# Kernel optimization log

Hardware: AMD Instinct MI355X
Metric: run time of the kernel (lower is better)

Reference implementation:

```python
import jax, jax.numpy as jnp
import numpy as np

B, GH, GW, F = 64, 7, 7, 1024  # batch, enc grid, feature_size (hardcoded 1024 in module)
A, E, H, V, T = 512, 512, 512, 30000, 20  # attention_dim, embed, hidden, vocab, max caption len


def setup_inputs() -> dict:
    key = jax.random.key(0)
    ks = jax.random.split(key, 20)
    s = 0.02
    features = jax.random.normal(ks[0], (B, GH, GW, F), jnp.float32)
    captions = jax.random.randint(ks[1], (B, T), 0, V)
    lengths = jax.random.randint(ks[2], (B,), 2, T + 1)
    lengths = lengths.at[0].set(T)  # ensure max(decode_lengths) == T-1 (static)
    inp = dict(features=features, captions=captions, lengths=lengths)
    inp["We"] = jax.random.normal(ks[3], (A, F), jnp.float32) * s   # attention.encoder_att
    inp["be"] = jnp.zeros((A,), jnp.float32)
    inp["Wd"] = jax.random.normal(ks[4], (A, H), jnp.float32) * s   # attention.decoder_att
    inp["bd"] = jnp.zeros((A,), jnp.float32)
    inp["Wf"] = jax.random.normal(ks[5], (1, A), jnp.float32) * s   # attention.full_att
    inp["bf"] = jnp.zeros((1,), jnp.float32)
    inp["emb"] = jax.random.uniform(ks[6], (V, E), jnp.float32, -0.1, 0.1)
    inp["Wih"] = jax.random.normal(ks[7], (3 * H, E + F), jnp.float32) * s  # GRUCell weight_ih
    inp["Whh"] = jax.random.normal(ks[8], (3 * H, H), jnp.float32) * s      # GRUCell weight_hh
    inp["bih"] = jnp.zeros((3 * H,), jnp.float32)
    inp["bhh"] = jnp.zeros((3 * H,), jnp.float32)
    inp["Winit"] = jax.random.normal(ks[9], (H, F), jnp.float32) * s  # init_h
    inp["binit"] = jnp.zeros((H,), jnp.float32)
    inp["Wbeta"] = jax.random.normal(ks[10], (F, H), jnp.float32) * s  # f_beta
    inp["bbeta"] = jnp.zeros((F,), jnp.float32)
    inp["Wfc"] = jax.random.uniform(ks[11], (V, H), jnp.float32, -0.1, 0.1)  # fc
    inp["bfc"] = jnp.zeros((V,), jnp.float32)
    return inp


def reference(features, captions, lengths, We, be, Wd, bd, Wf, bf, emb,
              Wih, Whh, bih, bhh, Winit, binit, Wbeta, bbeta, Wfc, bfc):
    b = features.shape[0]
    feats = features.reshape(b, -1, features.shape[-1])  # (B, P, F)
    sort_ind = jnp.argsort(-lengths)
    lengths_s = lengths[sort_ind]
    feats = feats[sort_ind]
    caps = captions[sort_ind]
    decode_lengths = lengths_s - 1
    Tm = captions.shape[1] - 1  # static max decode length (lengths max == T)

    embs = emb[caps]                                  # (B, T, E)
    h0 = feats.mean(axis=1) @ Winit.T + binit         # (B, H)
    att1 = feats @ We.T + be                          # (B, P, A), loop-invariant

    def step(h, xs):
        emb_t, active = xs  # (B,E), (B,)
        att2 = h @ Wd.T + bd                                  # (B, A)
        e = jax.nn.relu(att1 + att2[:, None, :]) @ Wf[0] + bf[0]  # (B, P)
        alpha = jax.nn.softmax(e, axis=1)
        awe = jnp.einsum('bpf,bp->bf', feats, alpha)          # (B, F)
        gate = jax.nn.sigmoid(h @ Wbeta.T + bbeta)
        x = jnp.concatenate([emb_t, gate * awe], axis=1)      # (B, E+F)
        gi = x @ Wih.T + bih
        gh = h @ Whh.T + bhh
        ir, iz, inn = jnp.split(gi, 3, axis=1)
        hr, hz, hn = jnp.split(gh, 3, axis=1)
        r = jax.nn.sigmoid(ir + hr)
        z = jax.nn.sigmoid(iz + hz)
        n = jnp.tanh(inn + r * hn)
        h_new = (1.0 - z) * n + z * h
        preds = h_new @ Wfc.T + bfc                           # dropout in eval = identity
        am = active[:, None]
        return jnp.where(am, h_new, h), (jnp.where(am, preds, 0.0), jnp.where(am, alpha, 0.0))

    ts = jnp.arange(Tm)
    active = ts[:, None] < decode_lengths[None, :]            # (Tm, B)
    emb_seq = jnp.swapaxes(embs[:, :Tm, :], 0, 1)             # (Tm, B, E)
    _, (preds, alphas) = jax.lax.scan(step, h0, (emb_seq, active))
    predictions = jnp.swapaxes(preds, 0, 1)                   # (B, Tm, V)
    alphas = jnp.swapaxes(alphas, 0, 1)                       # (B, Tm, P)
    return predictions, caps, decode_lengths, alphas, sort_ind
```

## Files before the change

### kernel.cpp

```cpp
#include <hip/hip_runtime.h>
#include <math.h>

typedef __attribute__((ext_vector_type(8))) short bf16x8;
typedef __attribute__((ext_vector_type(4))) float f32x4;

#define TM 19
#define NV 30000

__device__ __forceinline__ float bf2f(unsigned short u){
  union { unsigned int i; float f; } v; v.i = ((unsigned int)u) << 16; return v.f;
}
__device__ __forceinline__ unsigned short f2bf(float f){
  union { float f; unsigned int i; } v; v.f = f;
  unsigned int x = v.i;
  unsigned int r = (x + 0x7fffu + ((x >> 16) & 1u)) >> 16;
  return (unsigned short)r;
}

__global__ void k_sort(const int* __restrict__ lengths, const int* __restrict__ captions,
                       int* __restrict__ sort_ws, int* __restrict__ dl_ws, int* __restrict__ caps_ws,
                       float* __restrict__ out_caps, float* __restrict__ out_dl, float* __restrict__ out_sort){
  int b = threadIdx.x;
  __shared__ int len_s[64];
  len_s[b] = lengths[b];
  __syncthreads();
  int lb = len_s[b];
  int r = 0;
  for(int j = 0; j < 64; j++){
    int lj = len_s[j];
    r += (lj > lb) || (lj == lb && j < b);
  }
  sort_ws[r] = b;
  dl_ws[r] = lb - 1;
  out_sort[r] = (float)b;
  out_dl[r] = (float)(lb - 1);
  for(int tt = 0; tt < 20; tt++){
    int c = captions[b*20 + tt];
    caps_ws[r*20 + tt] = c;
    out_caps[r*20 + tt] = (float)c;
  }
}

__global__ void k_cvt4(const float4* __restrict__ src, ushort4* __restrict__ dst, int n4){
  int i = blockIdx.x*256 + threadIdx.x;
  if(i < n4){
    float4 v = src[i];
    ushort4 o; o.x = f2bf(v.x); o.y = f2bf(v.y); o.z = f2bf(v.z); o.w = f2bf(v.w);
    dst[i] = o;
  }
}

__global__ void k_feats(const float* __restrict__ feats, const int* __restrict__ sort_ws,
                        unsigned short* __restrict__ feats_bf){
  int rp = blockIdx.x;
  int r = rp / 49, p = rp % 49;
  int sb = sort_ws[r];
  const float* src = feats + ((size_t)sb*49 + p)*1024;
  unsigned short* dst = feats_bf + (size_t)rp*1024;
  int f = threadIdx.x*4;
  float4 v = *(const float4*)(src + f);
  ushort4 o; o.x = f2bf(v.x); o.y = f2bf(v.y); o.z = f2bf(v.z); o.w = f2bf(v.w);
  *(ushort4*)(dst + f) = o;
}

__global__ void k_featmean(const float* __restrict__ feats, const int* __restrict__ sort_ws,
                           float* __restrict__ fm){
  int r = blockIdx.x;
  int sb = sort_ws[r];
  const float* src = feats + (size_t)sb*49*1024;
  int f = threadIdx.x*4;
  float a0=0,a1=0,a2=0,a3=0;
  for(int p = 0; p < 49; p++){
    float4 v = *(const float4*)(src + p*1024 + f);
    a0 += v.x; a1 += v.y; a2 += v.z; a3 += v.w;
  }
  const float inv = 1.0f/49.0f;
  float4 o; o.x=a0*inv; o.y=a1*inv; o.z=a2*inv; o.w=a3*inv;
  *(float4*)(fm + r*1024 + f) = o;
}

__global__ void k_h0(const float* __restrict__ fm, const float* __restrict__ Winit,
                     const float* __restrict__ binit,
                     float* __restrict__ h, unsigned short* __restrict__ h_bf){
  int idx = blockIdx.x*256 + threadIdx.x;
  int r = idx >> 9, n = idx & 511;
  const float* a = fm + r*1024;
  const float* wrow = Winit + (size_t)n*1024;
  float s = 0.f;
  for(int k = 0; k < 1024; k += 4){
    float4 av = *(const float4*)(a + k);
    float4 wv = *(const float4*)(wrow + k);
    s += av.x*wv.x + av.y*wv.y + av.z*wv.z + av.w*wv.w;
  }
  s += binit[n];
  h[idx] = s;
  h_bf[idx] = f2bf(s);
}

__global__ void k_embs(const float* __restrict__ emb, const int* __restrict__ caps_ws,
                       unsigned short* __restrict__ embs_bf){
  int row = blockIdx.x;
  int t = row >> 6, r = row & 63;
  int cap = caps_ws[r*20 + t];
  const float* src = emb + (size_t)cap*512;
  unsigned short* dst = embs_bf + (size_t)row*512;
  int e = threadIdx.x*2;
  float2 v = *(const float2*)(src + e);
  dst[e]   = f2bf(v.x);
  dst[e+1] = f2bf(v.y);
}

__global__ __launch_bounds__(256) void k_gemm64(
    const unsigned short* __restrict__ A, int lda,
    const unsigned short* __restrict__ Bm, int ldb,
    float* __restrict__ C, int ldc, int Ksplit){
  __shared__ unsigned short As[64*40];
  __shared__ unsigned short Bs[64*40];
  int tid = threadIdx.x;
  int wave = tid >> 6, lane = tid & 63;
  int m0 = blockIdx.y*64, n0 = blockIdx.x*64;
  int k0 = blockIdx.z*Ksplit;
  int lrow = tid >> 2, lcol = (tid & 3)*8;
  const unsigned short* Ag = A + (size_t)(m0 + lrow)*lda + k0 + lcol;
  const unsigned short* Bg = Bm + (size_t)(n0 + lrow)*ldb + k0 + lcol;
  f32x4 acc0 = {0,0,0,0}, acc1 = {0,0,0,0}, acc2 = {0,0,0,0}, acc3 = {0,0,0,0};
  int quad = lane >> 4;
  int mrow = (wave << 4) + (lane & 15);
  for(int kk = 0; kk < Ksplit; kk += 32){
    uint4 av = *(const uint4*)(Ag + kk);
    uint4 bv = *(const uint4*)(Bg + kk);
    __syncthreads();
    *(uint4*)(&As[lrow*40 + lcol]) = av;
    *(uint4*)(&Bs[lrow*40 + lcol]) = bv;
    __syncthreads();
    bf16x8 a = *(const bf16x8*)(&As[mrow*40 + quad*8]);
    bf16x8 b0 = *(const bf16x8*)(&Bs[( 0 + (lane & 15))*40 + quad*8]);
    bf16x8 b1 = *(const bf16x8*)(&Bs[(16 + (lane & 15))*40 + quad*8]);
    bf16x8 b2 = *(const bf16x8*)(&Bs[(32 + (lane & 15))*40 + quad*8]);
    bf16x8 b3 = *(const bf16x8*)(&Bs[(48 + (lane & 15))*40 + quad*8]);
    acc0 = __builtin_amdgcn_mfma_f32_16x16x32_bf16(a, b0, acc0, 0, 0, 0);
    acc1 = __builtin_amdgcn_mfma_f32_16x16x32_bf16(a, b1, acc1, 0, 0, 0);
    acc2 = __builtin_amdgcn_mfma_f32_16x16x32_bf16(a, b2, acc2, 0, 0, 0);
    acc3 = __builtin_amdgcn_mfma_f32_16x16x32_bf16(a, b3, acc3, 0, 0, 0);
  }
  float* Cb = C + (size_t)blockIdx.z * ((size_t)gridDim.y*64*ldc);
  int col = lane & 15;
  #pragma unroll
  for(int rg = 0; rg < 4; rg++){
    int m = m0 + (wave << 4) + quad*4 + rg;
    float* crow = Cb + (size_t)m*ldc + n0 + col;
    crow[0]  = acc0[rg];
    crow[16] = acc1[rg];
    crow[32] = acc2[rg];
    crow[48] = acc3[rg];
  }
}

__global__ __launch_bounds__(256) void k_attn(
    const float* __restrict__ att1, const float* __restrict__ y1p,
    const float* __restrict__ bd, const float* __restrict__ be,
    const float* __restrict__ Wf, const float* __restrict__ bfb,
    const float* __restrict__ bbeta,
    const unsigned short* __restrict__ feats_bf,
    const int* __restrict__ dl_ws,
    unsigned short* __restrict__ x_awe, float* __restrict__ out_alph, int t){
  int r = blockIdx.x;
  int tid = threadIdx.x;
  __shared__ float att2s[512];
  __shared__ float es[64];
  __shared__ float alph[49];
  const float* y0 = y1p + (size_t)r*3072;
  const float* y1 = y1p + (size_t)64*3072 + (size_t)r*3072;
  for(int k = tid; k < 512; k += 256) att2s[k] = y0[k] + y1[k] + bd[k] + be[k];
  __syncthreads();
  int wave = tid >> 6, lane = tid & 63;
  for(int p = wave; p < 49; p += 4){
    const float* arow = att1 + ((size_t)r*49 + p)*512;
    float s = 0.f;
    #pragma unroll
    for(int i = 0; i < 8; i++){
      int k = lane + i*64;
      float v = arow[k] + att2s[k];
      s += fmaxf(v, 0.f) * Wf[k];
    }
    #pragma unroll
    for(int off = 32; off; off >>= 1) s += __shfl_xor(s, off, 64);
    if(lane == 0) es[p] = s + bfb[0];
  }
  __syncthreads();
  if(wave == 0){
    float v = (lane < 49) ? es[lane] : -1e30f;
    float m = v;
    #pragma unroll
    for(int off = 32; off; off >>= 1) m = fmaxf(m, __shfl_xor(m, off, 64));
    float ex = (lane < 49) ? __expf(v - m) : 0.f;
    float sm = ex;
    #pragma unroll
    for(int off = 32; off; off >>= 1) sm += __shfl_xor(sm, off, 64);
    float al = ex / sm;
    if(lane < 49){
      alph[lane] = al;
      bool act = t < dl_ws[r];
      out_alph[(size_t)r*(TM*49) + t*49 + lane] = act ? al : 0.f;
    }
  }
  __syncthreads();
  int f0 = tid*4;
  float a0=0,a1=0,a2=0,a3=0;
  const unsigned short* fr = feats_bf + (size_t)r*49*1024 + f0;
  for(int p = 0; p < 49; p++){
    float al = alph[p];
    ushort4 v = *(const ushort4*)(fr + p*1024);
    a0 += al*bf2f(v.x); a1 += al*bf2f(v.y); a2 += al*bf2f(v.z); a3 += al*bf2f(v.w);
  }
  const float* g0 = y0 + 512;
  const float* g1 = y1 + 512;
  ushort4 xo;
  float gp;
  gp = g0[f0+0] + g1[f0+0] + bbeta[f0+0]; xo.x = f2bf(a0 / (1.f + __expf(-gp)));
  gp = g0[f0+1] + g1[f0+1] + bbeta[f0+1]; xo.y = f2bf(a1 / (1.f + __expf(-gp)));
  gp = g0[f0+2] + g1[f0+2] + bbeta[f0+2]; xo.z = f2bf(a2 / (1.f + __expf(-gp)));
  gp = g0[f0+3] + g1[f0+3] + bbeta[f0+3]; xo.w = f2bf(a3 / (1.f + __expf(-gp)));
  *(ushort4*)(x_awe + (size_t)r*1024 + f0) = xo;
}

__global__ __launch_bounds__(256) void k_gru(
    const float* __restrict__ gi_emb, const float* __restrict__ gip,
    const float* __restrict__ y1p,
    const float* __restrict__ bih, const float* __restrict__ bhh,
    const int* __restrict__ dl_ws,
    float* __restrict__ h, unsigned short* __restrict__ h_bf,
    unsigned short* __restrict__ hseq, int t){
  int idx = blockIdx.x*256 + threadIdx.x;
  int r = idx >> 9, j = idx & 511;
  const float* ge = gi_emb + (size_t)(t*64 + r)*1536;
  float ir = ge[j], iz = ge[512 + j], in_ = ge[1024 + j];
  #pragma unroll
  for(int s = 0; s < 4; s++){
    const float* gp = gip + (size_t)s*64*1536 + (size_t)r*1536;
    ir += gp[j]; iz += gp[512 + j]; in_ += gp[1024 + j];
  }
  ir += bih[j]; iz += bih[512 + j]; in_ += bih[1024 + j];
  float hr = bhh[j], hz = bhh[512 + j], hn = bhh[1024 + j];
  #pragma unroll
  for(int s = 0; s < 2; s++){
    const float* yp = y1p + (size_t)s*64*3072 + (size_t)r*3072 + 1536;
    hr += yp[j]; hz += yp[512 + j]; hn += yp[1024 + j];
  }
  float rg = 1.f / (1.f + __expf(-(ir + hr)));
  float zg = 1.f / (1.f + __expf(-(iz + hz)));
  float ng = tanhf(in_ + rg*hn);
  float hold = h[idx];
  float hnew = (1.f - zg)*ng + zg*hold;
  hseq[(size_t)t*32768 + idx] = f2bf(hnew);
  bool act = t < dl_ws[r];
  float hout = act ? hnew : hold;
  h[idx] = hout;
  h_bf[idx] = f2bf(hout);
}

__global__ __launch_bounds__(256) void k_preds(
    const unsigned short* __restrict__ hseq, const unsigned short* __restrict__ Wfc_bf,
    const float* __restrict__ bfc, const int* __restrict__ dl_ws,
    float* __restrict__ out_pred){
  __shared__ unsigned short As[64*40];
  __shared__ unsigned short Bs[64*40];
  int tid = threadIdx.x;
  int wave = tid >> 6, lane = tid & 63;
  int m0 = blockIdx.y*64, n0 = blockIdx.x*64;
  int lrow = tid >> 2, lcol = (tid & 3)*8;
  const unsigned short* Ag = hseq + (size_t)(m0 + lrow)*512 + lcol;
  int brow = n0 + lrow;
  bool bvalid = brow < NV;
  const unsigned short* Bg = Wfc_bf + (size_t)(bvalid ? brow : 0)*512 + lcol;
  f32x4 acc0 = {0,0,0,0}, acc1 = {0,0,0,0}, acc2 = {0,0,0,0}, acc3 = {0,0,0,0};
  int quad = lane >> 4;
  int mrow = (wave << 4) + (lane & 15);
  for(int kk = 0; kk < 512; kk += 32){
    uint4 av = *(const uint4*)(Ag + kk);
    uint4 bv;
    if(bvalid) bv = *(const uint4*)(Bg + kk);
    else { bv.x = 0; bv.y = 0; bv.z = 0; bv.w = 0; }
    __syncthreads();
    *(uint4*)(&As[lrow*40 + lcol]) = av;
    *(uint4*)(&Bs[lrow*40 + lcol]) = bv;
    __syncthreads();
    bf16x8 a = *(const bf16x8*)(&As[mrow*40 + quad*8]);
    bf16x8 b0 = *(const bf16x8*)(&Bs[( 0 + (lane & 15))*40 + quad*8]);
    bf16x8 b1 = *(const bf16x8*)(&Bs[(16 + (lane & 15))*40 + quad*8]);
    bf16x8 b2 = *(const bf16x8*)(&Bs[(32 + (lane & 15))*40 + quad*8]);
    bf16x8 b3 = *(const bf16x8*)(&Bs[(48 + (lane & 15))*40 + quad*8]);
    acc0 = __builtin_amdgcn_mfma_f32_16x16x32_bf16(a, b0, acc0, 0, 0, 0);
    acc1 = __builtin_amdgcn_mfma_f32_16x16x32_bf16(a, b1, acc1, 0, 0, 0);
    acc2 = __builtin_amdgcn_mfma_f32_16x16x32_bf16(a, b2, acc2, 0, 0, 0);
    acc3 = __builtin_amdgcn_mfma_f32_16x16x32_bf16(a, b3, acc3, 0, 0, 0);
  }
  int col = lane & 15;
  #pragma unroll
  for(int j = 0; j < 4; j++){
    int n = n0 + j*16 + col;
    if(n < NV){
      float bias = bfc[n];
      f32x4 acc = (j == 0) ? acc0 : (j == 1) ? acc1 : (j == 2) ? acc2 : acc3;
      #pragma unroll
      for(int rg = 0; rg < 4; rg++){
        int mr = m0 + (wave << 4) + quad*4 + rg;
        int t = mr >> 6, r = mr & 63;
        bool act = t < dl_ws[r];
        float v = act ? (acc[rg] + bias) : 0.f;
        out_pred[(size_t)r*((size_t)TM*NV) + (size_t)t*NV + n] = v;
      }
    }
  }
}

extern "C" void kernel_launch(void* const* d_in, const int* in_sizes, int n_in,
                              void* d_out, int out_size, void* d_ws, size_t ws_size,
                              hipStream_t stream){
  const float* features = (const float*)d_in[0];
  const int*   captions = (const int*)d_in[1];
  const int*   lengths  = (const int*)d_in[2];
  const float* We    = (const float*)d_in[3];
  const float* be    = (const float*)d_in[4];
  const float* Wd    = (const float*)d_in[5];
  const float* bd    = (const float*)d_in[6];
  const float* Wf    = (const float*)d_in[7];
  const float* bfb   = (const float*)d_in[8];
  const float* emb   = (const float*)d_in[9];
  const float* Wih   = (const float*)d_in[10];
  const float* Whh   = (const float*)d_in[11];
  const float* bih   = (const float*)d_in[12];
  const float* bhh   = (const float*)d_in[13];
  const float* Winit = (const float*)d_in[14];
  const float* binit = (const float*)d_in[15];
  const float* Wbeta = (const float*)d_in[16];
  const float* bbeta = (const float*)d_in[17];
  const float* Wfc   = (const float*)d_in[18];
  const float* bfc   = (const float*)d_in[19];

  float* out = (float*)d_out;
  float* out_pred = out;
  float* out_caps = out + 36480000;
  float* out_dl   = out + 36481280;
  float* out_alph = out + 36481344;
  float* out_sort = out + 36540928;

  char* w = (char*)d_ws;
  auto alloc = [&](size_t bytes){ void* p = (void*)w; w += (bytes + 255) & ~(size_t)255; return p; };
  unsigned short* We_bf    = (unsigned short*)alloc((size_t)512*1024*2);
  unsigned short* W1_bf    = (unsigned short*)alloc((size_t)3072*512*2);
  unsigned short* Wih_bf   = (unsigned short*)alloc((size_t)1536*1536*2);
  unsigned short* Wfc_bf   = (unsigned short*)alloc((size_t)NV*512*2);
  unsigned short* feats_bf = (unsigned short*)alloc((size_t)64*49*1024*2);
  unsigned short* embs_bf  = (unsigned short*)alloc((size_t)1216*512*2);
  unsigned short* hseq_bf  = (unsigned short*)alloc((size_t)1216*512*2);
  unsigned short* h_bf     = (unsigned short*)alloc((size_t)64*512*2);
  unsigned short* xawe_bf  = (unsigned short*)alloc((size_t)64*1024*2);
  float* att1   = (float*)alloc((size_t)3136*512*4);
  float* gi_emb = (float*)alloc((size_t)1216*1536*4);
  float* y1p    = (float*)alloc((size_t)2*64*3072*4);
  float* gip    = (float*)alloc((size_t)4*64*1536*4);
  float* hbuf   = (float*)alloc((size_t)64*512*4);
  float* fmean  = (float*)alloc((size_t)64*1024*4);
  int* sort_ws  = (int*)alloc(64*4);
  int* dl_ws    = (int*)alloc(64*4);
  int* caps_ws  = (int*)alloc(1280*4);
  (void)in_sizes; (void)n_in; (void)out_size; (void)ws_size;

  k_sort<<<1, 64, 0, stream>>>(lengths, captions, sort_ws, dl_ws, caps_ws, out_caps, out_dl, out_sort);

  k_cvt4<<<512,  256, 0, stream>>>((const float4*)We,    (ushort4*)We_bf,             512*1024/4);
  k_cvt4<<<256,  256, 0, stream>>>((const float4*)Wd,    (ushort4*)W1_bf,             512*512/4);
  k_cvt4<<<512,  256, 0, stream>>>((const float4*)Wbeta, (ushort4*)(W1_bf + 512*512), 1024*512/4);
  k_cvt4<<<768,  256, 0, stream>>>((const float4*)Whh,   (ushort4*)(W1_bf + 1536*512),1536*512/4);
  k_cvt4<<<2304, 256, 0, stream>>>((const float4*)Wih,   (ushort4*)Wih_bf,            1536*1536/4);
  k_cvt4<<<15000,256, 0, stream>>>((const float4*)Wfc,   (ushort4*)Wfc_bf,            NV*512/4);

  k_feats<<<3136, 256, 0, stream>>>(features, sort_ws, feats_bf);
  k_featmean<<<64, 256, 0, stream>>>(features, sort_ws, fmean);
  k_h0<<<128, 256, 0, stream>>>(fmean, Winit, binit, hbuf, h_bf);
  k_embs<<<1216, 256, 0, stream>>>(emb, caps_ws, embs_bf);

  k_gemm64<<<dim3(8, 49, 1), 256, 0, stream>>>(feats_bf, 1024, We_bf, 1024, att1, 512, 1024);
  k_gemm64<<<dim3(24, 19, 1), 256, 0, stream>>>(embs_bf, 512, Wih_bf, 1536, gi_emb, 1536, 512);

  for(int t = 0; t < TM; t++){
    k_gemm64<<<dim3(48, 1, 2), 256, 0, stream>>>(h_bf, 512, W1_bf, 512, y1p, 3072, 256);
    k_attn<<<64, 256, 0, stream>>>(att1, y1p, bd, be, Wf, bfb, bbeta, feats_bf, dl_ws, xawe_bf, out_alph, t);
    k_gemm64<<<dim3(24, 1, 4), 256, 0, stream>>>(xawe_bf, 1024, Wih_bf + 512, 1536, gip, 1536, 256);
    k_gru<<<128, 256, 0, stream>>>(gi_emb, gip, y1p, bih, bhh, dl_ws, hbuf, h_bf, hseq_bf, t);
  }

  k_preds<<<dim3(469, 19, 1), 256, 0, stream>>>(hseq_bf, Wfc_bf, bfc, dl_ws, out_pred);
}
```

Before: 943.2 us.

## Fuse recurrent decode loop into one persistent kernel with grid barriers

Replaces the 76 per-timestep kernel launches (gemm, attention, gemm, GRU) with a single persistent kernel of 96 blocks. The blocks step through the four phases and sync at atomic-counter grid barriers. The goal is to remove launch overhead and inter-kernel gaps on the serial recurrence. The final prediction GEMM grid is also transposed so adjacent blocks share the same Wfc tile. The persistent kernel relies on all 96 blocks being co-resident, and leaves many blocks idle during the attention phase.

```diff
diff --git a/kernel.cpp b/kernel.cpp
--- a/kernel.cpp
+++ b/kernel.cpp
@@ -6,6 +6,7 @@
 
 #define TM 19
 #define NV 30000
+#define NB 96
 
 __device__ __forceinline__ float bf2f(unsigned short u){
   union { unsigned int i; float f; } v; v.i = ((unsigned int)u) << 16; return v.f;
@@ -17,10 +18,26 @@
   return (unsigned short)r;
 }
 
+__device__ __forceinline__ void gbar(int* cnt, int& phase){
+  __syncthreads();
+  if(threadIdx.x == 0){
+    phase++;
+    __threadfence();
+    __hip_atomic_fetch_add(cnt, 1, __ATOMIC_RELEASE, __HIP_MEMORY_SCOPE_AGENT);
+    while(__hip_atomic_load(cnt, __ATOMIC_ACQUIRE, __HIP_MEMORY_SCOPE_AGENT) < NB*phase){
+      __builtin_amdgcn_s_sleep(1);
+    }
+    __threadfence();
+  }
+  __syncthreads();
+}
+
 __global__ void k_sort(const int* __restrict__ lengths, const int* __restrict__ captions,
                        int* __restrict__ sort_ws, int* __restrict__ dl_ws, int* __restrict__ caps_ws,
-                       float* __restrict__ out_caps, float* __restrict__ out_dl, float* __restrict__ out_sort){
+                       float* __restrict__ out_caps, float* __restrict__ out_dl, float* __restrict__ out_sort,
+                       int* __restrict__ cnt){
   int b = threadIdx.x;
+  if(b == 0) *cnt = 0;
   __shared__ int len_s[64];
   len_s[b] = lengths[b];
   __syncthreads();
@@ -110,25 +127,22 @@
   dst[e+1] = f2bf(v.y);
 }
 
-__global__ __launch_bounds__(256) void k_gemm64(
+__device__ __forceinline__ void gemm64_dev(
     const unsigned short* __restrict__ A, int lda,
-    const unsigned short* __restrict__ Bm, int ldb,
-    float* __restrict__ C, int ldc, int Ksplit){
-  __shared__ unsigned short As[64*40];
-  __shared__ unsigned short Bs[64*40];
+    const unsigned short* __restrict__ B, int ldb,
+    float* __restrict__ C, int ldc, int kiters,
+    unsigned short* As, unsigned short* Bs){
   int tid = threadIdx.x;
   int wave = tid >> 6, lane = tid & 63;
-  int m0 = blockIdx.y*64, n0 = blockIdx.x*64;
-  int k0 = blockIdx.z*Ksplit;
   int lrow = tid >> 2, lcol = (tid & 3)*8;
-  const unsigned short* Ag = A + (size_t)(m0 + lrow)*lda + k0 + lcol;
-  const unsigned short* Bg = Bm + (size_t)(n0 + lrow)*ldb + k0 + lcol;
+  const unsigned short* Ag = A + (size_t)lrow*lda + lcol;
+  const unsigned short* Bg = B + (size_t)lrow*ldb + lcol;
   f32x4 acc0 = {0,0,0,0}, acc1 = {0,0,0,0}, acc2 = {0,0,0,0}, acc3 = {0,0,0,0};
   int quad = lane >> 4;
   int mrow = (wave << 4) + (lane & 15);
-  for(int kk = 0; kk < Ksplit; kk += 32){
-    uint4 av = *(const uint4*)(Ag + kk);
-    uint4 bv = *(const uint4*)(Bg + kk);
+  for(int it = 0; it < kiters; it++){
+    uint4 av = *(const uint4*)(Ag + it*32);
+    uint4 bv = *(const uint4*)(Bg + it*32);
     __syncthreads();
     *(uint4*)(&As[lrow*40 + lcol]) = av;
     *(uint4*)(&Bs[lrow*40 + lcol]) = bv;
@@ -143,12 +157,11 @@
     acc2 = __builtin_amdgcn_mfma_f32_16x16x32_bf16(a, b2, acc2, 0, 0, 0);
     acc3 = __builtin_amdgcn_mfma_f32_16x16x32_bf16(a, b3, acc3, 0, 0, 0);
   }
-  float* Cb = C + (size_t)blockIdx.z * ((size_t)gridDim.y*64*ldc);
   int col = lane & 15;
   #pragma unroll
   for(int rg = 0; rg < 4; rg++){
-    int m = m0 + (wave << 4) + quad*4 + rg;
-    float* crow = Cb + (size_t)m*ldc + n0 + col;
+    int m = (wave << 4) + quad*4 + rg;
+    float* crow = C + (size_t)m*ldc + col;
     crow[0]  = acc0[rg];
     crow[16] = acc1[rg];
     crow[32] = acc2[rg];
@@ -156,107 +169,143 @@
   }
 }
 
-__global__ __launch_bounds__(256) void k_attn(
-    const float* __restrict__ att1, const float* __restrict__ y1p,
-    const float* __restrict__ bd, const float* __restrict__ be,
-    const float* __restrict__ Wf, const float* __restrict__ bfb,
-    const float* __restrict__ bbeta,
-    const unsigned short* __restrict__ feats_bf,
-    const int* __restrict__ dl_ws,
-    unsigned short* __restrict__ x_awe, float* __restrict__ out_alph, int t){
-  int r = blockIdx.x;
+__global__ __launch_bounds__(256) void k_gemm64(
+    const unsigned short* __restrict__ A, int lda,
+    const unsigned short* __restrict__ Bm, int ldb,
+    float* __restrict__ C, int ldc, int Ksplit){
+  __shared__ unsigned short As[64*40];
+  __shared__ unsigned short Bs[64*40];
+  int m0 = blockIdx.y*64, n0 = blockIdx.x*64;
+  int k0 = blockIdx.z*Ksplit;
+  float* Cb = C + (size_t)blockIdx.z * ((size_t)gridDim.y*64*ldc);
+  gemm64_dev(A + (size_t)m0*lda + k0, lda, Bm + (size_t)n0*ldb + k0, ldb,
+             Cb + (size_t)m0*ldc + n0, ldc, Ksplit/32, As, Bs);
+}
+
+__global__ __launch_bounds__(256) void k_loop(
+    const float* __restrict__ att1, const float* __restrict__ bd, const float* __restrict__ be,
+    const float* __restrict__ Wf, const float* __restrict__ bfb, const float* __restrict__ bbeta,
+    const unsigned short* __restrict__ feats_bf, const int* __restrict__ dl_ws,
+    const unsigned short* __restrict__ W1_bf, const unsigned short* __restrict__ Wih_bf,
+    const float* __restrict__ gi_emb, const float* __restrict__ bih, const float* __restrict__ bhh,
+    float* __restrict__ y1p, float* __restrict__ gip,
+    unsigned short* __restrict__ xawe_bf,
+    float* __restrict__ h, unsigned short* __restrict__ h_bf, unsigned short* __restrict__ hseq,
+    float* __restrict__ out_alph, int* cnt){
+  __shared__ __align__(16) char smbuf[10240];
+  unsigned short* As = (unsigned short*)smbuf;
+  unsigned short* Bs = (unsigned short*)(smbuf + 5120);
+  float* att2s = (float*)smbuf;
+  float* es    = (float*)(smbuf + 2048);
+  float* alph  = (float*)(smbuf + 2304);
+  int blk = blockIdx.x;
   int tid = threadIdx.x;
-  __shared__ float att2s[512];
-  __shared__ float es[64];
-  __shared__ float alph[49];
-  const float* y0 = y1p + (size_t)r*3072;
-  const float* y1 = y1p + (size_t)64*3072 + (size_t)r*3072;
-  for(int k = tid; k < 512; k += 256) att2s[k] = y0[k] + y1[k] + bd[k] + be[k];
-  __syncthreads();
-  int wave = tid >> 6, lane = tid & 63;
-  for(int p = wave; p < 49; p += 4){
-    const float* arow = att1 + ((size_t)r*49 + p)*512;
-    float s = 0.f;
-    #pragma unroll
-    for(int i = 0; i < 8; i++){
-      int k = lane + i*64;
-      float v = arow[k] + att2s[k];
-      s += fmaxf(v, 0.f) * Wf[k];
-    }
-    #pragma unroll
-    for(int off = 32; off; off >>= 1) s += __shfl_xor(s, off, 64);
-    if(lane == 0) es[p] = s + bfb[0];
-  }
-  __syncthreads();
-  if(wave == 0){
-    float v = (lane < 49) ? es[lane] : -1e30f;
-    float m = v;
-    #pragma unroll
-    for(int off = 32; off; off >>= 1) m = fmaxf(m, __shfl_xor(m, off, 64));
-    float ex = (lane < 49) ? __expf(v - m) : 0.f;
-    float sm = ex;
-    #pragma unroll
-    for(int off = 32; off; off >>= 1) sm += __shfl_xor(sm, off, 64);
-    float al = ex / sm;
-    if(lane < 49){
-      alph[lane] = al;
+  int phase = 0;
+
+  for(int t = 0; t < TM; t++){
+    {
+      int tile = blk % 48, ks = blk / 48;
+      int n0 = tile*64, k0 = ks*256;
+      gemm64_dev(h_bf + k0, 512, W1_bf + (size_t)n0*512 + k0, 512,
+                 y1p + (size_t)ks*64*3072 + n0, 3072, 8, As, Bs);
+    }
+    gbar(cnt, phase);
+
+    if(blk < 64){
+      int r = blk;
+      int wave = tid >> 6, lane = tid & 63;
+      const float* y0 = y1p + (size_t)r*3072;
+      const float* y1 = y1p + (size_t)64*3072 + (size_t)r*3072;
+      for(int k = tid; k < 512; k += 256) att2s[k] = y0[k] + y1[k] + bd[k] + be[k];
+      __syncthreads();
+      for(int p = wave; p < 49; p += 4){
+        const float* arow = att1 + ((size_t)r*49 + p)*512;
+        float s = 0.f;
+        #pragma unroll
+        for(int i = 0; i < 8; i++){
+          int k = lane + i*64;
+          float v = arow[k] + att2s[k];
+          s += fmaxf(v, 0.f) * Wf[k];
+        }
+        #pragma unroll
+        for(int off = 32; off; off >>= 1) s += __shfl_xor(s, off, 64);
+        if(lane == 0) es[p] = s + bfb[0];
+      }
+      __syncthreads();
+      if(wave == 0){
+        float v = (lane < 49) ? es[lane] : -1e30f;
+        float m = v;
+        #pragma unroll
+        for(int off = 32; off; off >>= 1) m = fmaxf(m, __shfl_xor(m, off, 64));
+        float ex = (lane < 49) ? __expf(v - m) : 0.f;
+        float sm = ex;
+        #pragma unroll
+        for(int off = 32; off; off >>= 1) sm += __shfl_xor(sm, off, 64);
+        float al = ex / sm;
+        if(lane < 49){
+          alph[lane] = al;
+          bool act = t < dl_ws[r];
+          out_alph[(size_t)r*(TM*49) + t*49 + lane] = act ? al : 0.f;
+        }
+      }
+      __syncthreads();
+      int f0 = tid*4;
+      float a0=0,a1=0,a2=0,a3=0;
+      const unsigned short* fr = feats_bf + (size_t)r*49*1024 + f0;
+      for(int p = 0; p < 49; p++){
+        float al = alph[p];
+        ushort4 v = *(const ushort4*)(fr + p*1024);
+        a0 += al*bf2f(v.x); a1 += al*bf2f(v.y); a2 += al*bf2f(v.z); a3 += al*bf2f(v.w);
+      }
+      const float* g0 = y0 + 512;
+      const float* g1 = y1 + 512;
+      ushort4 xo;
+      float gp;
+      gp = g0[f0+0] + g1[f0+0] + bbeta[f0+0]; xo.x = f2bf(a0 / (1.f + __expf(-gp)));
+      gp = g0[f0+1] + g1[f0+1] + bbeta[f0+1]; xo.y = f2bf(a1 / (1.f + __expf(-gp)));
+      gp = g0[f0+2] + g1[f0+2] + bbeta[f0+2]; xo.z = f2bf(a2 / (1.f + __expf(-gp)));
+      gp = g0[f0+3] + g1[f0+3] + bbeta[f0+3]; xo.w = f2bf(a3 / (1.f + __expf(-gp)));
+      *(ushort4*)(xawe_bf + (size_t)r*1024 + f0) = xo;
+    }
+    gbar(cnt, phase);
+
+    {
+      int tile = blk % 24, ks = blk / 24;
+      int n0 = tile*64, k0 = ks*256;
+      gemm64_dev(xawe_bf + k0, 1024, Wih_bf + 512 + (size_t)n0*1536 + k0, 1536,
+                 gip + (size_t)ks*64*1536 + n0, 1536, 8, As, Bs);
+    }
+    gbar(cnt, phase);
+
+    for(int idx = blk*256 + tid; idx < 32768; idx += NB*256){
+      int r = idx >> 9, j = idx & 511;
+      const float* ge = gi_emb + (size_t)(t*64 + r)*1536;
+      float ir = ge[j], iz = ge[512 + j], in_ = ge[1024 + j];
+      #pragma unroll
+      for(int s = 0; s < 4; s++){
+        const float* gp = gip + (size_t)s*64*1536 + (size_t)r*1536;
+        ir += gp[j]; iz += gp[512 + j]; in_ += gp[1024 + j];
+      }
+      ir += bih[j]; iz += bih[512 + j]; in_ += bih[1024 + j];
+      float hr = bhh[j], hz = bhh[512 + j], hn = bhh[1024 + j];
+      #pragma unroll
+      for(int s = 0; s < 2; s++){
+        const float* yp = y1p + (size_t)s*64*3072 + (size_t)r*3072 + 1536;
+        hr += yp[j]; hz += yp[512 + j]; hn += yp[1024 + j];
+      }
+      float rg = 1.f / (1.f + __expf(-(ir + hr)));
+      float zg = 1.f / (1.f + __expf(-(iz + hz)));
+      float ng = tanhf(in_ + rg*hn);
+      float hold = h[idx];
+      float hnew = (1.f - zg)*ng + zg*hold;
+      hseq[(size_t)t*32768 + idx] = f2bf(hnew);
       bool act = t < dl_ws[r];
-      out_alph[(size_t)r*(TM*49) + t*49 + lane] = act ? al : 0.f;
-    }
-  }
-  __syncthreads();
-  int f0 = tid*4;
-  float a0=0,a1=0,a2=0,a3=0;
-  const unsigned short* fr = feats_bf + (size_t)r*49*1024 + f0;
-  for(int p = 0; p < 49; p++){
-    float al = alph[p];
-    ushort4 v = *(const ushort4*)(fr + p*1024);
-    a0 += al*bf2f(v.x); a1 += al*bf2f(v.y); a2 += al*bf2f(v.z); a3 += al*bf2f(v.w);
-  }
-  const float* g0 = y0 + 512;
-  const float* g1 = y1 + 512;
-  ushort4 xo;
-  float gp;
-  gp = g0[f0+0] + g1[f0+0] + bbeta[f0+0]; xo.x = f2bf(a0 / (1.f + __expf(-gp)));
-  gp = g0[f0+1] + g1[f0+1] + bbeta[f0+1]; xo.y = f2bf(a1 / (1.f + __expf(-gp)));
-  gp = g0[f0+2] + g1[f0+2] + bbeta[f0+2]; xo.z = f2bf(a2 / (1.f + __expf(-gp)));
-  gp = g0[f0+3] + g1[f0+3] + bbeta[f0+3]; xo.w = f2bf(a3 / (1.f + __expf(-gp)));
-  *(ushort4*)(x_awe + (size_t)r*1024 + f0) = xo;
-}
-
-__global__ __launch_bounds__(256) void k_gru(
-    const float* __restrict__ gi_emb, const float* __restrict__ gip,
-    const float* __restrict__ y1p,
-    const float* __restrict__ bih, const float* __restrict__ bhh,
-    const int* __restrict__ dl_ws,
-    float* __restrict__ h, unsigned short* __restrict__ h_bf,
-    unsigned short* __restrict__ hseq, int t){
-  int idx = blockIdx.x*256 + threadIdx.x;
-  int r = idx >> 9, j = idx & 511;
-  const float* ge = gi_emb + (size_t)(t*64 + r)*1536;
-  float ir = ge[j], iz = ge[512 + j], in_ = ge[1024 + j];
-  #pragma unroll
-  for(int s = 0; s < 4; s++){
-    const float* gp = gip + (size_t)s*64*1536 + (size_t)r*1536;
-    ir += gp[j]; iz += gp[512 + j]; in_ += gp[1024 + j];
-  }
-  ir += bih[j]; iz += bih[512 + j]; in_ += bih[1024 + j];
-  float hr = bhh[j], hz = bhh[512 + j], hn = bhh[1024 + j];
-  #pragma unroll
-  for(int s = 0; s < 2; s++){
-    const float* yp = y1p + (size_t)s*64*3072 + (size_t)r*3072 + 1536;
-    hr += yp[j]; hz += yp[512 + j]; hn += yp[1024 + j];
-  }
-  float rg = 1.f / (1.f + __expf(-(ir + hr)));
-  float zg = 1.f / (1.f + __expf(-(iz + hz)));
-  float ng = tanhf(in_ + rg*hn);
-  float hold = h[idx];
-  float hnew = (1.f - zg)*ng + zg*hold;
-  hseq[(size_t)t*32768 + idx] = f2bf(hnew);
-  bool act = t < dl_ws[r];
-  float hout = act ? hnew : hold;
-  h[idx] = hout;
-  h_bf[idx] = f2bf(hout);
+      float hout = act ? hnew : hold;
+      h[idx] = hout;
+      h_bf[idx] = f2bf(hout);
+    }
+    gbar(cnt, phase);
+  }
 }
 
 __global__ __launch_bounds__(256) void k_preds(
@@ -267,7 +316,7 @@
   __shared__ unsigned short Bs[64*40];
   int tid = threadIdx.x;
   int wave = tid >> 6, lane = tid & 63;
-  int m0 = blockIdx.y*64, n0 = blockIdx.x*64;
+  int m0 = blockIdx.x*64, n0 = blockIdx.y*64;
   int lrow = tid >> 2, lcol = (tid & 3)*8;
   const unsigned short* Ag = hseq + (size_t)(m0 + lrow)*512 + lcol;
   int brow = n0 + lrow;
@@ -365,9 +414,10 @@
   int* sort_ws  = (int*)alloc(64*4);
   int* dl_ws    = (int*)alloc(64*4);
   int* caps_ws  = (int*)alloc(1280*4);
+  int* cnt      = (int*)alloc(256);
   (void)in_sizes; (void)n_in; (void)out_size; (void)ws_size;
 
-  k_sort<<<1, 64, 0, stream>>>(lengths, captions, sort_ws, dl_ws, caps_ws, out_caps, out_dl, out_sort);
+  k_sort<<<1, 64, 0, stream>>>(lengths, captions, sort_ws, dl_ws, caps_ws, out_caps, out_dl, out_sort, cnt);
 
   k_cvt4<<<512,  256, 0, stream>>>((const float4*)We,    (ushort4*)We_bf,             512*1024/4);
   k_cvt4<<<256,  256, 0, stream>>>((const float4*)Wd,    (ushort4*)W1_bf,             512*512/4);
@@ -384,12 +434,9 @@
   k_gemm64<<<dim3(8, 49, 1), 256, 0, stream>>>(feats_bf, 1024, We_bf, 1024, att1, 512, 1024);
   k_gemm64<<<dim3(24, 19, 1), 256, 0, stream>>>(embs_bf, 512, Wih_bf, 1536, gi_emb, 1536, 512);
 
-  for(int t = 0; t < TM; t++){
-    k_gemm64<<<dim3(48, 1, 2), 256, 0, stream>>>(h_bf, 512, W1_bf, 512, y1p, 3072, 256);
-    k_attn<<<64, 256, 0, stream>>>(att1, y1p, bd, be, Wf, bfb, bbeta, feats_bf, dl_ws, xawe_bf, out_alph, t);
-    k_gemm64<<<dim3(24, 1, 4), 256, 0, stream>>>(xawe_bf, 1024, Wih_bf + 512, 1536, gip, 1536, 256);
-    k_gru<<<128, 256, 0, stream>>>(gi_emb, gip, y1p, bih, bhh, dl_ws, hbuf, h_bf, hseq_bf, t);
-  }
-
-  k_preds<<<dim3(469, 19, 1), 256, 0, stream>>>(hseq_bf, Wfc_bf, bfc, dl_ws, out_pred);
-}
+  k_loop<<<NB, 256, 0, stream>>>(att1, bd, be, Wf, bfb, bbeta, feats_bf, dl_ws,
+                                 W1_bf, Wih_bf, gi_emb, bih, bhh,
+                                 y1p, gip, xawe_bf, hbuf, h_bf, hseq_bf, out_alph, cnt);
+
+  k_preds<<<dim3(19, 469, 1), 256, 0, stream>>>(hseq_bf, Wfc_bf, bfc, dl_ws, out_pred);
+}
```

Result: slower. 1.682 ms (+78.3%).
